# Kernel tuning notes

Measured on AMD Instinct MI355X. Metric: run time of the kernel, lower is better.

Reference implementation:

```python
import jax, jax.numpy as jnp
import numpy as np

B, C, H, W = 16, 512, 64, 64


def setup_inputs() -> dict:
    key = jax.random.key(0)
    ks = jax.random.split(key, 5)
    s = 0.02  # init scale for projection weights
    return {
        "x": jax.random.normal(ks[0], (B, C, H, W), jnp.float32),
        "Wqkv": jax.random.normal(ks[1], (3 * C, C), jnp.float32) * s,
        "bqkv": jnp.zeros((3 * C,), jnp.float32),
        "Wm": jax.random.normal(ks[2], (2 * C, C), jnp.float32) * s,
        "bm": jnp.zeros((2 * C,), jnp.float32),
        "Wg": jax.random.normal(ks[3], (C, 2 * C), jnp.float32) * s,
        "bg": jnp.zeros((C,), jnp.float32),
        "Wr": jax.random.normal(ks[4], (C, C), jnp.float32) * s,
        "br": jnp.zeros((C,), jnp.float32),
    }


def reference(x, Wqkv, bqkv, Wm, bm, Wg, bg, Wr, br):
    b, c, h, w = x.shape
    n = h * w
    xf = x.reshape(b, c, n)  # [B,C,N]
    # qkv projection: [B,3C,N] -> q,k,v each [B,C,N]
    qkv = jnp.einsum('oc,bcn->bon', Wqkv, xf) + bqkv[None, :, None]
    q, k, v = qkv[:, :c], qkv[:, c:2 * c], qkv[:, 2 * c:]
    # modulation from v: mq, mk each [B,C,N]
    mqk = jnp.einsum('oc,bcn->bon', Wm, v) + bm[None, :, None]
    mq, mk = mqk[:, :c], mqk[:, c:]
    _q = jax.nn.softmax(-jax.nn.relu(q * mq), axis=-1)   # softmax over N
    _k = jax.nn.relu(k * mk)                             # [B,C,N]
    # channel attention: [B,C,N] @ [B,N,C] -> [B,C,C]
    scores = jnp.einsum('bcn,bdn->bcd', _q, _k) / jnp.sqrt(jnp.float32(c))
    attn = jax.nn.softmax(scores, axis=-1)
    y = jnp.einsum('bcd,bdn->bcn', attn, v)              # [B,C,N]
    y2d = y.reshape(b, c, h, w)
    # gated residual: g = sigmoid(W_g @ cat(y, x))
    catf = jnp.concatenate([y, xf], axis=1)              # [B,2C,N]
    g = jax.nn.sigmoid(jnp.einsum('oc,bcn->bon', Wg, catf) + bg[None, :, None]).reshape(b, c, h, w)
    r = (jnp.einsum('oc,bcn->bon', Wr, xf) + br[None, :, None]).reshape(b, c, h, w)
    out = g * r + (1.0 - g) * y2d
    return (out, attn)
```

## Files before the change

kernel.cpp:

```cpp
#include <hip/hip_runtime.h>
#include <math.h>

#define Bb 16
#define Cc 512
#define Nn 4096
#define CN (512L * 4096)

typedef __bf16 bf16x8 __attribute__((ext_vector_type(8)));
typedef float  floatx4 __attribute__((ext_vector_type(4)));

__device__ __forceinline__ unsigned short f2bf(float f) {
    unsigned int u = __float_as_uint(f);
    unsigned int r = (u + 0x7FFFu + ((u >> 16) & 1u)) >> 16;
    return (unsigned short)r;
}
__device__ __forceinline__ float bf2f(unsigned short s) {
    return __uint_as_float(((unsigned int)s) << 16);
}

__device__ __forceinline__ void gload16(const void* g, void* l) {
    __builtin_amdgcn_global_load_lds(
        (const __attribute__((address_space(1))) unsigned int*)g,
        (__attribute__((address_space(3))) unsigned int*)l,
        16, 0, 0);
}

__device__ __forceinline__ void xcd_swizzle(int& bx, int& by, int& bz) {
    const int nwg  = gridDim.x * gridDim.y * gridDim.z;
    const int orig = blockIdx.x + gridDim.x * (blockIdx.y + gridDim.y * blockIdx.z);
    const int q8   = nwg >> 3, r8 = nwg & 7;
    const int xcd  = orig & 7, sub_i = orig >> 3;
    const int logical = (xcd < r8 ? xcd * (q8 + 1) : r8 * (q8 + 1) + (xcd - r8) * q8) + sub_i;
    bx = logical % gridDim.x;
    const int btmp = logical / gridDim.x;
    by = btmp % gridDim.y;
    bz = btmp / gridDim.y;
}

template<int OUTF32, int SPLIT>
__global__ __launch_bounds__(512) void gemm_bt256(
    const unsigned short* __restrict__ A1,
    const unsigned short* __restrict__ A2, int lda, int asplit,
    const unsigned short* __restrict__ B, int ldb,
    const float* __restrict__ bias,
    void* __restrict__ Cv, int ldc,
    int K, float scale,
    long sA, long sB, long sC)
{
    __shared__ __align__(16) unsigned short Alds[2][32 * 512];
    __shared__ __align__(16) unsigned short Blds[2][32 * 512];

    int bx, by, bz;
    xcd_swizzle(bx, by, bz);

    const int t    = threadIdx.x;
    const int lane = t & 63;
    const int wave = t >> 6;
    const int m0 = by * 256;
    const int n0 = bx * 256;
    const int wm = (wave >> 2) * 128;
    const int wn = (wave & 3) * 64;

    const unsigned short* Ab1 = A1 + (size_t)bz * sA;
    const unsigned short* Ab2 = SPLIT ? (A2 + (size_t)bz * sA) : nullptr;
    const unsigned short* Bb_ = B + (size_t)bz * sB;

    const int srow = lane & 15;
    const int sk8  = (lane >> 4) * 8;
    const ptrdiff_t sjump = SPLIT ? (Ab2 - Ab1) - (ptrdiff_t)asplit : 0;

    const unsigned short* gA[4];
    const unsigned short* gB[4];
#pragma unroll
    for (int u = 0; u < 4; ++u) {
        int si = wave * 4 + u;
        int rowsub = si >> 1, kh = si & 1;
        gA[u] = Ab1 + (size_t)(m0 + rowsub * 16 + srow) * lda + kh * 32 + sk8;
        gB[u] = Bb_ + (size_t)(n0 + rowsub * 16 + srow) * ldb + kh * 32 + sk8;
    }

    auto stage = [&](int buf, int k0) {
        const bool hi = SPLIT && (k0 >= asplit);
#pragma unroll
        for (int u = 0; u < 4; ++u) {
            int si = wave * 4 + u;
            const unsigned short* a = gA[u] + k0;
            if (hi) a += sjump;
            gload16(a,          &Alds[buf][si * 512]);
            gload16(gB[u] + k0, &Blds[buf][si * 512]);
        }
    };

    floatx4 acc[8][4] = {};

    const int nt = K >> 6;
    stage(0, 0);
    int cur = 0;

    for (int ti = 0; ti < nt; ++ti) {
        if (ti + 1 < nt) {
            stage(cur ^ 1, (ti + 1) << 6);
            asm volatile("s_waitcnt vmcnt(8)" ::: "memory");
        } else {
            asm volatile("s_waitcnt vmcnt(0)" ::: "memory");
        }
        __builtin_amdgcn_s_barrier();
        __builtin_amdgcn_sched_barrier(0);

        const int ra = wm >> 4;
        const int rb = wn >> 4;
#pragma unroll
        for (int s = 0; s < 2; ++s) {
            bf16x8 af[8], bfr[4];
#pragma unroll
            for (int i = 0; i < 8; ++i)
                af[i] = *(const bf16x8*)&Alds[cur][((ra + i) * 2 + s) * 512 + lane * 8];
#pragma unroll
            for (int j = 0; j < 4; ++j)
                bfr[j] = *(const bf16x8*)&Blds[cur][((rb + j) * 2 + s) * 512 + lane * 8];
            __builtin_amdgcn_s_setprio(1);
#pragma unroll
            for (int i = 0; i < 8; ++i)
#pragma unroll
                for (int j = 0; j < 4; ++j)
                    acc[i][j] = __builtin_amdgcn_mfma_f32_16x16x32_bf16(af[i], bfr[j], acc[i][j], 0, 0, 0);
            __builtin_amdgcn_s_setprio(0);
        }

        asm volatile("s_waitcnt lgkmcnt(0)" ::: "memory");
        __builtin_amdgcn_s_barrier();
        __builtin_amdgcn_sched_barrier(0);
        cur ^= 1;
    }

    const int rbase = (lane >> 4) * 4;
    const int cofs  = lane & 15;
    if (OUTF32) {
        float* C = (float*)Cv + (size_t)bz * sC;
#pragma unroll
        for (int j = 0; j < 4; ++j) {
            int col = n0 + wn + j * 16 + cofs;
            float bv = bias ? bias[col] : 0.0f;
#pragma unroll
            for (int i = 0; i < 8; ++i)
#pragma unroll
                for (int r = 0; r < 4; ++r) {
                    int row = m0 + wm + i * 16 + rbase + r;
                    C[(size_t)row * ldc + col] = acc[i][j][r] * scale + bv;
                }
        }
    } else {
        unsigned short* C = (unsigned short*)Cv + (size_t)bz * sC;
        float* sbuf = (float*)&Alds[0][0] + wave * (16 * 68);
        float bvj[4];
#pragma unroll
        for (int j = 0; j < 4; ++j)
            bvj[j] = bias ? bias[n0 + wn + j * 16 + cofs] : 0.0f;
        const int rrow = lane >> 2;
        const int rcg  = (lane & 3) * 16;
        unsigned short* cbase = C + (size_t)(m0 + wm + rrow) * ldc + (n0 + wn + rcg);
#pragma unroll
        for (int i = 0; i < 8; ++i) {
#pragma unroll
            for (int j = 0; j < 4; ++j)
#pragma unroll
                for (int r = 0; r < 4; ++r)
                    sbuf[(rbase + r) * 68 + j * 16 + cofs] = acc[i][j][r] * scale + bvj[j];
            unsigned short* cp = cbase + (size_t)i * 16 * ldc;
            {
                float4 w0 = *(const float4*)&sbuf[rrow * 68 + rcg + 0];
                float4 w1 = *(const float4*)&sbuf[rrow * 68 + rcg + 4];
                uint4 o0;
                o0.x = (unsigned)f2bf(w0.x) | ((unsigned)f2bf(w0.y) << 16);
                o0.y = (unsigned)f2bf(w0.z) | ((unsigned)f2bf(w0.w) << 16);
                o0.z = (unsigned)f2bf(w1.x) | ((unsigned)f2bf(w1.y) << 16);
                o0.w = (unsigned)f2bf(w1.z) | ((unsigned)f2bf(w1.w) << 16);
                *(uint4*)cp = o0;
            }
            {
                float4 w2 = *(const float4*)&sbuf[rrow * 68 + rcg + 8];
                float4 w3 = *(const float4*)&sbuf[rrow * 68 + rcg + 12];
                uint4 o1;
                o1.x = (unsigned)f2bf(w2.x) | ((unsigned)f2bf(w2.y) << 16);
                o1.y = (unsigned)f2bf(w2.z) | ((unsigned)f2bf(w2.w) << 16);
                o1.z = (unsigned)f2bf(w3.x) | ((unsigned)f2bf(w3.y) << 16);
                o1.w = (unsigned)f2bf(w3.z) | ((unsigned)f2bf(w3.w) << 16);
                *(uint4*)(cp + 8) = o1;
            }
        }
    }
}

template<int OUTF32, int SPLIT>
__global__ __launch_bounds__(256) void gemm_bt(
    const unsigned short* __restrict__ A1,
    const unsigned short* __restrict__ A2, int lda, int asplit,
    const unsigned short* __restrict__ B, int ldb,
    const float* __restrict__ bias,
    void* __restrict__ Cv, int ldc,
    int K, float scale,
    long sA, long sB, long sC)
{
    __shared__ __align__(16) unsigned short Alds[3][8 * 512];
    __shared__ __align__(16) unsigned short Blds[3][8 * 512];

    int bx, by, bz;
    xcd_swizzle(bx, by, bz);

    const int t    = threadIdx.x;
    const int lane = t & 63;
    const int wave = t >> 6;
    const int m0 = by * 128;
    const int n0 = bx * 128;
    const int wm = (wave >> 1) * 64;
    const int wn = (wave & 1) * 64;

    const unsigned short* Ab1 = A1 + (size_t)bz * sA;
    const unsigned short* Ab2 = SPLIT ? (A2 + (size_t)bz * sA) : nullptr;
    const unsigned short* Bb_ = B + (size_t)bz * sB;

    const int srow = lane & 15;
    const int sk   = (lane >> 4) * 8;
    const int sub0 = wave * 2;

    const unsigned short* gA0 = Ab1 + (size_t)(m0 + (sub0    ) * 16 + srow) * lda + sk;
    const unsigned short* gA1 = Ab1 + (size_t)(m0 + (sub0 + 1) * 16 + srow) * lda + sk;
    const unsigned short* gB0 = Bb_ + (size_t)(n0 + (sub0    ) * 16 + srow) * ldb + sk;
    const unsigned short* gB1 = Bb_ + (size_t)(n0 + (sub0 + 1) * 16 + srow) * ldb + sk;
    const ptrdiff_t sjump = SPLIT ? (Ab2 - Ab1) - (ptrdiff_t)asplit : 0;

    auto stage = [&](int buf, int k0) {
        const unsigned short* a0 = gA0 + k0;
        const unsigned short* a1 = gA1 + k0;
        if (SPLIT && k0 >= asplit) { a0 += sjump; a1 += sjump; }
        gload16(a0,       &Alds[buf][(sub0    ) * 512]);
        gload16(gB0 + k0, &Blds[buf][(sub0    ) * 512]);
        gload16(a1,       &Alds[buf][(sub0 + 1) * 512]);
        gload16(gB1 + k0, &Blds[buf][(sub0 + 1) * 512]);
    };

    floatx4 acc[4][4] = {};

    const int nt = K >> 5;
    stage(0, 0);
    if (nt > 1) stage(1, 32);
    int cur = 0;

    for (int ti = 0; ti < nt; ++ti) {
        if (ti + 2 < nt) {
            int bufn = cur + 2; if (bufn >= 3) bufn -= 3;
            stage(bufn, (ti + 2) << 5);
            asm volatile("s_waitcnt vmcnt(8)" ::: "memory");
        } else if (ti + 1 < nt) {
            asm volatile("s_waitcnt vmcnt(4)" ::: "memory");
        } else {
            asm volatile("s_waitcnt vmcnt(0)" ::: "memory");
        }
        __builtin_amdgcn_s_barrier();
        __builtin_amdgcn_sched_barrier(0);

        bf16x8 af[4], bfr[4];
#pragma unroll
        for (int i = 0; i < 4; ++i) {
            af[i]  = *(const bf16x8*)&Alds[cur][((wm >> 4) + i) * 512 + lane * 8];
            bfr[i] = *(const bf16x8*)&Blds[cur][((wn >> 4) + i) * 512 + lane * 8];
        }
        __builtin_amdgcn_s_setprio(1);
#pragma unroll
        for (int i = 0; i < 4; ++i)
#pragma unroll
            for (int j = 0; j < 4; ++j)
                acc[i][j] = __builtin_amdgcn_mfma_f32_16x16x32_bf16(af[i], bfr[j], acc[i][j], 0, 0, 0);
        __builtin_amdgcn_s_setprio(0);

        asm volatile("s_waitcnt lgkmcnt(0)" ::: "memory");
        __builtin_amdgcn_s_barrier();
        __builtin_amdgcn_sched_barrier(0);
        cur = (cur == 2) ? 0 : cur + 1;
    }

    const int rbase = (lane >> 4) * 4;
    const int cofs  = lane & 15;
#pragma unroll
    for (int j = 0; j < 4; ++j) {
        int col = n0 + wn + j * 16 + cofs;
        float bv = bias ? bias[col] : 0.0f;
#pragma unroll
        for (int i = 0; i < 4; ++i) {
#pragma unroll
            for (int r = 0; r < 4; ++r) {
                int row = m0 + wm + i * 16 + rbase + r;
                float v = acc[i][j][r] * scale + bv;
                if (OUTF32) {
                    float* C = (float*)Cv + (size_t)bz * sC;
                    C[(size_t)row * ldc + col] = v;
                } else {
                    unsigned short* C = (unsigned short*)Cv + (size_t)bz * sC;
                    C[(size_t)row * ldc + col] = f2bf(v);
                }
            }
        }
    }
}

__global__ __launch_bounds__(256) void wcast(const float* __restrict__ w,
                                             unsigned short* __restrict__ o, int n)
{
    int i = (blockIdx.x * 256 + threadIdx.x) * 4;
    float4 v = *(const float4*)&w[i];
    ushort4 u;
    u.x = f2bf(v.x); u.y = f2bf(v.y); u.z = f2bf(v.z); u.w = f2bf(v.w);
    *(ushort4*)&o[i] = u;
}

__global__ __launch_bounds__(256) void transpose_x(const float* __restrict__ x,
                                                   unsigned short* __restrict__ xp)
{
    __shared__ unsigned short tile[64][65];
    const float* X = x + (size_t)blockIdx.z * CN;
    unsigned short* O = xp + (size_t)blockIdx.z * CN;
    int n0 = blockIdx.x * 64, c0 = blockIdx.y * 64;
    int tq = (threadIdx.x & 15) * 4, tr = threadIdx.x >> 4;
#pragma unroll
    for (int r = 0; r < 4; ++r) {
        int cl = tr + r * 16;
        float4 v = *(const float4*)&X[(size_t)(c0 + cl) * 4096 + n0 + tq];
        tile[tq + 0][cl] = f2bf(v.x);
        tile[tq + 1][cl] = f2bf(v.y);
        tile[tq + 2][cl] = f2bf(v.z);
        tile[tq + 3][cl] = f2bf(v.w);
    }
    __syncthreads();
#pragma unroll
    for (int r = 0; r < 4; ++r) {
        int nl = tr + r * 16;
        ushort4 o;
        o.x = tile[nl][tq + 0]; o.y = tile[nl][tq + 1];
        o.z = tile[nl][tq + 2]; o.w = tile[nl][tq + 3];
        *(ushort4*)&O[(size_t)(n0 + nl) * 512 + c0 + tq] = o;
    }
}

__global__ __launch_bounds__(256) void qk_transform(
    const unsigned short* __restrict__ qkv, const unsigned short* __restrict__ mqk,
    unsigned short* __restrict__ T, int coff, int neg)
{
    __shared__ __align__(8) unsigned short tile[64][68];
    const unsigned short* S1 = qkv + (size_t)blockIdx.z * (4096L * 1536) + coff;
    const unsigned short* S2 = mqk + (size_t)blockIdx.z * (4096L * 1024) + coff;
    unsigned short* O = T + (size_t)blockIdx.z * CN;
    int n0 = blockIdx.x * 64, c0 = blockIdx.y * 64;
    int tq = (threadIdx.x & 15) * 4, tr = threadIdx.x >> 4;
#pragma unroll
    for (int r = 0; r < 4; ++r) {
        int nl = tr + r * 16;
        ushort4 a = *(const ushort4*)&S1[(size_t)(n0 + nl) * 1536 + c0 + tq];
        ushort4 m = *(const ushort4*)&S2[(size_t)(n0 + nl) * 1024 + c0 + tq];
        float f0 = fmaxf(bf2f(a.x) * bf2f(m.x), 0.0f);
        float f1 = fmaxf(bf2f(a.y) * bf2f(m.y), 0.0f);
        float f2 = fmaxf(bf2f(a.z) * bf2f(m.z), 0.0f);
        float f3 = fmaxf(bf2f(a.w) * bf2f(m.w), 0.0f);
        if (neg) { f0 = -f0; f1 = -f1; f2 = -f2; f3 = -f3; }
        ushort4 p;
        p.x = f2bf(f0); p.y = f2bf(f1); p.z = f2bf(f2); p.w = f2bf(f3);
        *(ushort4*)&tile[nl][tq] = p;
    }
    __syncthreads();
#pragma unroll
    for (int r = 0; r < 4; ++r) {
        int cl = tr + r * 16;
        ushort4 o;
        o.x = tile[tq + 0][cl]; o.y = tile[tq + 1][cl];
        o.z = tile[tq + 2][cl]; o.w = tile[tq + 3][cl];
        *(ushort4*)&O[(size_t)(c0 + cl) * 4096 + n0 + tq] = o;
    }
}

__global__ __launch_bounds__(256) void qsoftmax_bf(unsigned short* __restrict__ Q)
{
    unsigned short* p = Q + (size_t)blockIdx.x * 4096;
    const int t = threadIdx.x;
    const int lane = t & 63;
    const int wv = t >> 6;
    __shared__ float red[8];

    float vals[16];
    float mx = -1e30f;
#pragma unroll
    for (int i = 0; i < 16; ++i) {
        float v = bf2f(p[t + i * 256]);
        vals[i] = v;
        mx = fmaxf(mx, v);
    }
#pragma unroll
    for (int off = 32; off > 0; off >>= 1) mx = fmaxf(mx, __shfl_xor(mx, off));
    if (lane == 0) red[wv] = mx;
    __syncthreads();
    mx = fmaxf(fmaxf(red[0], red[1]), fmaxf(red[2], red[3]));

    float sum = 0.0f;
#pragma unroll
    for (int i = 0; i < 16; ++i) {
        vals[i] = __expf(vals[i] - mx);
        sum += vals[i];
    }
#pragma unroll
    for (int off = 32; off > 0; off >>= 1) sum += __shfl_xor(sum, off);
    if (lane == 0) red[4 + wv] = sum;
    __syncthreads();
    sum = red[4] + red[5] + red[6] + red[7];
    float inv = 1.0f / sum;
#pragma unroll
    for (int i = 0; i < 16; ++i) p[t + i * 256] = f2bf(vals[i] * inv);
}

__global__ __launch_bounds__(256) void attn_softmax_dual(
    float* __restrict__ attnf, unsigned short* __restrict__ attnb)
{
    float* p = attnf + (size_t)blockIdx.x * 512;
    unsigned short* pb = attnb + (size_t)blockIdx.x * 512;
    const int t = threadIdx.x;
    const int lane = t & 63;
    const int wv = t >> 6;
    __shared__ float red[8];

    float v0 = p[t], v1 = p[t + 256];
    float mx = fmaxf(v0, v1);
#pragma unroll
    for (int off = 32; off > 0; off >>= 1) mx = fmaxf(mx, __shfl_xor(mx, off));
    if (lane == 0) red[wv] = mx;
    __syncthreads();
    mx = fmaxf(fmaxf(red[0], red[1]), fmaxf(red[2], red[3]));

    float e0 = __expf(v0 - mx);
    float e1 = __expf(v1 - mx);
    float sum = e0 + e1;
#pragma unroll
    for (int off = 32; off > 0; off >>= 1) sum += __shfl_xor(sum, off);
    if (lane == 0) red[4 + wv] = sum;
    __syncthreads();
    sum = red[4] + red[5] + red[6] + red[7];
    float inv = 1.0f / sum;
    float a0 = e0 * inv, a1 = e1 * inv;
    p[t] = a0;        p[t + 256] = a1;
    pb[t] = f2bf(a0); pb[t + 256] = f2bf(a1);
}

__global__ __launch_bounds__(256) void final_fuse(
    const unsigned short* __restrict__ gl, const unsigned short* __restrict__ rr,
    const unsigned short* __restrict__ yy, float* __restrict__ out)
{
    __shared__ __align__(16) float tile[64][68];
    size_t bo = (size_t)blockIdx.z * CN;
    const unsigned short* G_ = gl + bo;
    const unsigned short* R_ = rr + bo;
    const unsigned short* Y_ = yy + bo;
    float* O = out + bo;
    int n0 = blockIdx.x * 64, c0 = blockIdx.y * 64;
    int tq = (threadIdx.x & 15) * 4, tr = threadIdx.x >> 4;
#pragma unroll
    for (int r = 0; r < 4; ++r) {
        int nl = tr + r * 16;
        size_t base = (size_t)(n0 + nl) * 512 + c0 + tq;
        ushort4 g4 = *(const ushort4*)&G_[base];
        ushort4 r4 = *(const ushort4*)&R_[base];
        ushort4 y4 = *(const ushort4*)&Y_[base];
        float4 o;
        float g;
        g = 1.0f / (1.0f + __expf(-bf2f(g4.x))); o.x = g * bf2f(r4.x) + (1.0f - g) * bf2f(y4.x);
        g = 1.0f / (1.0f + __expf(-bf2f(g4.y))); o.y = g * bf2f(r4.y) + (1.0f - g) * bf2f(y4.y);
        g = 1.0f / (1.0f + __expf(-bf2f(g4.z))); o.z = g * bf2f(r4.z) + (1.0f - g) * bf2f(y4.z);
        g = 1.0f / (1.0f + __expf(-bf2f(g4.w))); o.w = g * bf2f(r4.w) + (1.0f - g) * bf2f(y4.w);
        *(float4*)&tile[nl][tq] = o;
    }
    __syncthreads();
#pragma unroll
    for (int r = 0; r < 4; ++r) {
        int cl = tr + r * 16;
        float4 o;
        o.x = tile[tq + 0][cl]; o.y = tile[tq + 1][cl];
        o.z = tile[tq + 2][cl]; o.w = tile[tq + 3][cl];
        *(float4*)&O[(size_t)(c0 + cl) * 4096 + n0 + tq] = o;
    }
}

extern "C" void kernel_launch(void* const* d_in, const int* in_sizes, int n_in,
                              void* d_out, int out_size, void* d_ws, size_t ws_size,
                              hipStream_t stream)
{
    const float* x    = (const float*)d_in[0];
    const float* Wqkv = (const float*)d_in[1];
    const float* bqkv = (const float*)d_in[2];
    const float* Wm   = (const float*)d_in[3];
    const float* bm   = (const float*)d_in[4];
    const float* Wg   = (const float*)d_in[5];
    const float* bg   = (const float*)d_in[6];
    const float* Wr   = (const float*)d_in[7];
    const float* br   = (const float*)d_in[8];

    float* out      = (float*)d_out;
    float* attn_all = out + (size_t)Bb * CN;

    unsigned short* wq_bf = (unsigned short*)d_ws;
    unsigned short* wm_bf = wq_bf + 1536 * 512;
    unsigned short* wg_bf = wm_bf + 1024 * 512;
    unsigned short* wr_bf = wg_bf + 512 * 1024;
    unsigned short* dyn   = wr_bf + 512 * 512;
    const size_t fixed_bytes = (size_t)(1536 * 512 + 1024 * 512 + 512 * 1024 + 512 * 512) * 2;
    const size_t per_batch_bytes = (size_t)4096 * 4096 * 2;

    int G = 16;
    while (G > 1 && fixed_bytes + (size_t)G * per_batch_bytes > ws_size) G >>= 1;

    dim3 blk(256);
    dim3 blk512(512);
    const float inv_sqrt_c = 0.044194173824159216f;

    wcast<<<1536 * 512 / 1024, blk, 0, stream>>>(Wqkv, wq_bf, 1536 * 512);
    wcast<<<1024 * 512 / 1024, blk, 0, stream>>>(Wm,   wm_bf, 1024 * 512);
    wcast<<<512 * 1024 / 1024, blk, 0, stream>>>(Wg,   wg_bf, 512 * 1024);
    wcast<<<512 * 512  / 1024, blk, 0, stream>>>(Wr,   wr_bf, 512 * 512);

    for (int b0 = 0; b0 < Bb; b0 += G) {
        unsigned short* xp   = dyn;
        unsigned short* qkvp = xp   + (size_t)G * 4096 * 512;
        unsigned short* mqkp = qkvp + (size_t)G * 4096 * 1536;
        unsigned short* qp   = mqkp + (size_t)G * 4096 * 1024;
        unsigned short* kp   = qp   + (size_t)G * CN;
        unsigned short* yp   = mqkp;
        unsigned short* glp  = mqkp + (size_t)G * CN;
        unsigned short* rp   = qp;
        unsigned short* abf  = kp;

        const float* xg   = x + (size_t)b0 * CN;
        float* outg       = out + (size_t)b0 * CN;
        float* attng      = attn_all + (size_t)b0 * 512 * 512;

        transpose_x<<<dim3(64, 8, G), blk, 0, stream>>>(xg, xp);

        gemm_bt256<0, 0><<<dim3(6, 16, G), blk512, 0, stream>>>(
            xp, nullptr, 512, 0, wq_bf, 512, bqkv, qkvp, 1536,
            512, 1.0f, 4096L * 512, 0L, 4096L * 1536);

        gemm_bt256<0, 0><<<dim3(4, 16, G), blk512, 0, stream>>>(
            qkvp + 1024, nullptr, 1536, 0, wm_bf, 512, bm, mqkp, 1024,
            512, 1.0f, 4096L * 1536, 0L, 4096L * 1024);

        qk_transform<<<dim3(64, 8, G), blk, 0, stream>>>(qkvp, mqkp, qp, 0, 1);
        qk_transform<<<dim3(64, 8, G), blk, 0, stream>>>(qkvp, mqkp, kp, 512, 0);

        qsoftmax_bf<<<G * 512, blk, 0, stream>>>(qp);

        gemm_bt<1, 0><<<dim3(4, 4, G), blk, 0, stream>>>(
            qp, nullptr, 4096, 0, kp, 4096, nullptr, attng, 512,
            4096, inv_sqrt_c, CN, CN, 512L * 512);

        attn_softmax_dual<<<G * 512, blk, 0, stream>>>(attng, abf);

        gemm_bt256<0, 0><<<dim3(2, 16, G), blk512, 0, stream>>>(
            qkvp + 1024, nullptr, 1536, 0, abf, 512, nullptr, yp, 512,
            512, 1.0f, 4096L * 1536, 512L * 512, 4096L * 512);

        gemm_bt256<0, 1><<<dim3(2, 16, G), blk512, 0, stream>>>(
            yp, xp, 512, 512, wg_bf, 1024, bg, glp, 512,
            1024, 1.0f, 4096L * 512, 0L, 4096L * 512);

        gemm_bt256<0, 0><<<dim3(2, 16, G), blk512, 0, stream>>>(
            xp, nullptr, 512, 0, wr_bf, 512, br, rp, 512,
            512, 1.0f, 4096L * 512, 0L, 4096L * 512);

        final_fuse<<<dim3(64, 8, G), blk, 0, stream>>>(glp, rp, yp, outg);
    }
}
```

Measured before the change: 1.099 ms.

## Interleave next-tile global loads with MFMA quarter-steps in GEMM main loop

Splits each K-tile's MFMA work into four quarter phases and spreads the four global-to-LDS staging units for the next tile across those phases, rather than issuing them all up front. This aims to overlap memory traffic with compute and lower register pressure by holding only 4 A fragments at a time. In exchange it adds extra block barriers per tile, which can introduce synchronisation stalls.

```diff
diff --git a/kernel.cpp b/kernel.cpp
--- a/kernel.cpp
+++ b/kernel.cpp
@@ -79,54 +79,94 @@
         gB[u] = Bb_ + (size_t)(n0 + rowsub * 16 + srow) * ldb + kh * 32 + sk8;
     }
 
-    auto stage = [&](int buf, int k0) {
-        const bool hi = SPLIT && (k0 >= asplit);
-#pragma unroll
-        for (int u = 0; u < 4; ++u) {
-            int si = wave * 4 + u;
-            const unsigned short* a = gA[u] + k0;
-            if (hi) a += sjump;
-            gload16(a,          &Alds[buf][si * 512]);
-            gload16(gB[u] + k0, &Blds[buf][si * 512]);
-        }
+    auto stage_unit = [&](int buf, int k0, int u) {
+        const unsigned short* a = gA[u] + k0;
+        if (SPLIT && k0 >= asplit) a += sjump;
+        int si = wave * 4 + u;
+        gload16(a,          &Alds[buf][si * 512]);
+        gload16(gB[u] + k0, &Blds[buf][si * 512]);
     };
 
     floatx4 acc[8][4] = {};
 
     const int nt = K >> 6;
-    stage(0, 0);
+    stage_unit(0, 0, 0); stage_unit(0, 0, 1);
+    stage_unit(0, 0, 2); stage_unit(0, 0, 3);
     int cur = 0;
 
+    const int ra = wm >> 4;
+    const int rb = wn >> 4;
+
     for (int ti = 0; ti < nt; ++ti) {
-        if (ti + 1 < nt) {
-            stage(cur ^ 1, (ti + 1) << 6);
-            asm volatile("s_waitcnt vmcnt(8)" ::: "memory");
+        const int kn = (ti + 1) << 6;
+        const bool more = (ti + 1 < nt);
+        bf16x8 af[4], bfr[4];
+
+        if (more) {
+            stage_unit(cur ^ 1, kn, 0); stage_unit(cur ^ 1, kn, 1);
+            asm volatile("s_waitcnt vmcnt(4)" ::: "memory");
         } else {
             asm volatile("s_waitcnt vmcnt(0)" ::: "memory");
         }
         __builtin_amdgcn_s_barrier();
         __builtin_amdgcn_sched_barrier(0);
-
-        const int ra = wm >> 4;
-        const int rb = wn >> 4;
-#pragma unroll
-        for (int s = 0; s < 2; ++s) {
-            bf16x8 af[8], bfr[4];
-#pragma unroll
-            for (int i = 0; i < 8; ++i)
-                af[i] = *(const bf16x8*)&Alds[cur][((ra + i) * 2 + s) * 512 + lane * 8];
+#pragma unroll
+        for (int j = 0; j < 4; ++j)
+            bfr[j] = *(const bf16x8*)&Blds[cur][((rb + j) * 2 + 0) * 512 + lane * 8];
+#pragma unroll
+        for (int i = 0; i < 4; ++i)
+            af[i] = *(const bf16x8*)&Alds[cur][((ra + i) * 2 + 0) * 512 + lane * 8];
+        __builtin_amdgcn_s_setprio(1);
+#pragma unroll
+        for (int i = 0; i < 4; ++i)
 #pragma unroll
             for (int j = 0; j < 4; ++j)
-                bfr[j] = *(const bf16x8*)&Blds[cur][((rb + j) * 2 + s) * 512 + lane * 8];
-            __builtin_amdgcn_s_setprio(1);
-#pragma unroll
-            for (int i = 0; i < 8; ++i)
-#pragma unroll
-                for (int j = 0; j < 4; ++j)
-                    acc[i][j] = __builtin_amdgcn_mfma_f32_16x16x32_bf16(af[i], bfr[j], acc[i][j], 0, 0, 0);
-            __builtin_amdgcn_s_setprio(0);
-        }
-
+                acc[i][j] = __builtin_amdgcn_mfma_f32_16x16x32_bf16(af[i], bfr[j], acc[i][j], 0, 0, 0);
+        __builtin_amdgcn_s_setprio(0);
+        __builtin_amdgcn_s_barrier();
+        __builtin_amdgcn_sched_barrier(0);
+
+        if (more) stage_unit(cur ^ 1, kn, 2);
+#pragma unroll
+        for (int i = 0; i < 4; ++i)
+            af[i] = *(const bf16x8*)&Alds[cur][((ra + 4 + i) * 2 + 0) * 512 + lane * 8];
+        __builtin_amdgcn_s_setprio(1);
+#pragma unroll
+        for (int i = 0; i < 4; ++i)
+#pragma unroll
+            for (int j = 0; j < 4; ++j)
+                acc[4 + i][j] = __builtin_amdgcn_mfma_f32_16x16x32_bf16(af[i], bfr[j], acc[4 + i][j], 0, 0, 0);
+        __builtin_amdgcn_s_setprio(0);
+        __builtin_amdgcn_s_barrier();
+        __builtin_amdgcn_sched_barrier(0);
+
+        if (more) stage_unit(cur ^ 1, kn, 3);
+#pragma unroll
+        for (int j = 0; j < 4; ++j)
+            bfr[j] = *(const bf16x8*)&Blds[cur][((rb + j) * 2 + 1) * 512 + lane * 8];
+#pragma unroll
+        for (int i = 0; i < 4; ++i)
+            af[i] = *(const bf16x8*)&Alds[cur][((ra + i) * 2 + 1) * 512 + lane * 8];
+        __builtin_amdgcn_s_setprio(1);
+#pragma unroll
+        for (int i = 0; i < 4; ++i)
+#pragma unroll
+            for (int j = 0; j < 4; ++j)
+                acc[i][j] = __builtin_amdgcn_mfma_f32_16x16x32_bf16(af[i], bfr[j], acc[i][j], 0, 0, 0);
+        __builtin_amdgcn_s_setprio(0);
+        __builtin_amdgcn_s_barrier();
+        __builtin_amdgcn_sched_barrier(0);
+
+#pragma unroll
+        for (int i = 0; i < 4; ++i)
+            af[i] = *(const bf16x8*)&Alds[cur][((ra + 4 + i) * 2 + 1) * 512 + lane * 8];
+        __builtin_amdgcn_s_setprio(1);
+#pragma unroll
+        for (int i = 0; i < 4; ++i)
+#pragma unroll
+            for (int j = 0; j < 4; ++j)
+                acc[4 + i][j] = __builtin_amdgcn_mfma_f32_16x16x32_bf16(af[i], bfr[j], acc[4 + i][j], 0, 0, 0);
+        __builtin_amdgcn_s_setprio(0);
         asm volatile("s_waitcnt lgkmcnt(0)" ::: "memory");
         __builtin_amdgcn_s_barrier();
         __builtin_amdgcn_sched_barrier(0);
```

Result: slower. 1.178 ms (+7.2%).
